# Optimization experiments

Measured on AMD Instinct MI355X. Metric: run time of the kernel, lower is better.

## Reference

```python
import jax, jax.numpy as jnp
import numpy as np

H = 8       # n_heads
N = 128     # n_vars
HEAD = 64   # per-head dim (== __init__ dim)


def setup_inputs() -> dict:
    key = jax.random.key(0)
    k0, k1, k2, k3, k4 = jax.random.split(key, 5)
    B, L = 4, 8192
    D = H * HEAD
    x = jax.random.normal(k0, (B, L, D), dtype=jnp.float32)
    # nn.Linear default init: U(-1/sqrt(fan_in), 1/sqrt(fan_in)), fan_in = HEAD
    s = 1.0 / np.sqrt(HEAD)
    w1 = jax.random.uniform(k1, (HEAD, HEAD), jnp.float32, -s, s)
    b1 = jax.random.uniform(k2, (HEAD,), jnp.float32, -s, s)
    w2 = jax.random.uniform(k3, (HEAD, HEAD), jnp.float32, -s, s)
    b2 = jax.random.uniform(k4, (HEAD,), jnp.float32, -s, s)
    return {"x": x, "w1": w1, "b1": b1, "w2": w2, "b2": b2}


def reference(x, w1, b1, w2, b2):
    B, L, D = x.shape
    P = L // N  # patches per variable
    # (B,L,D) -> (B,H,L,HEAD) -> (B,H,N,P,HEAD)
    xh = x.reshape(B, L, H, HEAD).transpose(0, 2, 1, 3).reshape(B, H, N, P, HEAD)
    q = xh @ w1.T + b1  # proj_1
    k = xh @ w2.T + b2  # proj_2
    # per (b,h,patch) NxN adjacency over variables
    adj = jax.nn.gelu(jnp.einsum('bhixd,bhjxd->bhxij', q, k), approximate=False)
    adj = jax.nn.softmax(adj, axis=-1)
    # dropout is identity in eval mode; F.normalize(p=1): divide by max(L1, eps)
    adj = adj / jnp.maximum(jnp.sum(jnp.abs(adj), axis=-1, keepdims=True), 1e-12)
    out = jnp.einsum('bhxij,bhjxd->bixhd', adj, xh)  # (B,N,P,H,HEAD)
    return out.reshape(B, L, H * HEAD)
```

## Files before the change

kernel.cpp:

```cpp
#include <hip/hip_runtime.h>
#include <math.h>


namespace {
constexpr int H = 8, NV = 128, HEAD = 64, B = 4, L = 8192;
constexpr int P = L / NV;
constexpr int D = H * HEAD;
constexpr int RS = P * D;
constexpr int NT2 = (B * H * P) / 2;

constexpr int XT_S = 136;
constexpr int XH_S = 72;
constexpr int TA_S = 72;

typedef _Float16 half8  __attribute__((ext_vector_type(8)));
typedef _Float16 half4h __attribute__((ext_vector_type(4)));
typedef _Float16 half2v __attribute__((ext_vector_type(2)));
typedef __fp16   fp16x2 __attribute__((ext_vector_type(2)));
typedef float    floatx4 __attribute__((ext_vector_type(4)));

__device__ __forceinline__ floatx4 mfma16(half8 a, half8 b, floatx4 c) {
    return __builtin_amdgcn_mfma_f32_16x16x32_f16(a, b, c, 0, 0, 0);
}

__device__ __forceinline__ half8 cvt8(float4 a, float4 b) {
    fp16x2 p0 = __builtin_amdgcn_cvt_pkrtz(a.x, a.y);
    fp16x2 p1 = __builtin_amdgcn_cvt_pkrtz(a.z, a.w);
    fp16x2 p2 = __builtin_amdgcn_cvt_pkrtz(b.x, b.y);
    fp16x2 p3 = __builtin_amdgcn_cvt_pkrtz(b.z, b.w);
    half8 r;
    r[0] = (_Float16)p0[0]; r[1] = (_Float16)p0[1];
    r[2] = (_Float16)p1[0]; r[3] = (_Float16)p1[1];
    r[4] = (_Float16)p2[0]; r[5] = (_Float16)p2[1];
    r[6] = (_Float16)p3[0]; r[7] = (_Float16)p3[1];
    return r;
}

__device__ __forceinline__ float& vslot(_Float16* xt, int j) {
    return ((float*)(xt + (size_t)(j >> 2) * XT_S + 128))[j & 3];
}

__global__ __launch_bounds__(256) void pack_g(
    const float* __restrict__ w1, const float* __restrict__ w2,
    const float* __restrict__ b1, const float* __restrict__ b2,
    _Float16* __restrict__ gth, float* __restrict__ g1f,
    float* __restrict__ g2f, float* __restrict__ cf)
{
    const int t = threadIdx.x;
    if (blockIdx.x == 16) {
        if (t < 64) {
            float a = 0.f;
            #pragma unroll 8
            for (int n = 0; n < 64; ++n) a = fmaf(w1[n * 64 + t], b2[n], a);
            g1f[t] = a;
        } else if (t < 128) {
            const int d = t - 64;
            float a = 0.f;
            #pragma unroll 8
            for (int n = 0; n < 64; ++n) a = fmaf(w2[n * 64 + d], b1[n], a);
            g2f[d] = a;
        } else if (t == 128) {
            float a = 0.f;
            for (int n = 0; n < 64; ++n) a = fmaf(b1[n], b2[n], a);
            cf[0] = a;
        }
        return;
    }
    const int gid = blockIdx.x * 256 + t;
    const int d = gid & 63, e = gid >> 6;
    float a = 0.f;
    #pragma unroll 8
    for (int n = 0; n < 64; ++n) a = fmaf(w1[n * 64 + d], w2[n * 64 + e], a);
    gth[e * 64 + d] = (_Float16)a;
}

__global__ __launch_bounds__(256, 3) void space_graph_mfma8(
    const float* __restrict__ x, const _Float16* __restrict__ gth,
    const float* __restrict__ g1f, const float* __restrict__ g2f,
    const float* __restrict__ cf, float* __restrict__ out)
{
    __shared__ _Float16 lds[64 * XT_S + NV * XH_S + NV * TA_S];
    _Float16* Xt = lds;
    _Float16* Xh = lds + 64 * XT_S;
    _Float16* TA = Xh + NV * XH_S;

    const int t    = threadIdx.x;
    const int lane = t & 63;
    const int w    = t >> 6;
    const int col  = lane & 15;
    const int quad = lane >> 4;
    const int c    = t & 15;
    const int ttv  = t >> 4;

    const int blk = blockIdx.x;
    const int ti0 = blk, ti1 = blk + NT2;
    const size_t base0 =
        ((size_t)(ti0 >> 9) * L + (size_t)(ti0 & (P - 1))) * D + (size_t)((ti0 >> 6) & (H - 1)) * HEAD;
    const size_t base1 =
        ((size_t)(ti1 >> 9) * L + (size_t)(ti1 & (P - 1))) * D + (size_t)((ti1 >> 6) & (H - 1)) * HEAD;

    float4 pf[8];
    #pragma unroll
    for (int it = 0; it < 4; ++it) {
        const int j0 = 2 * (ttv + 16 * it);
        pf[2 * it]     = *(const float4*)(x + base0 + (size_t)j0 * RS + c * 4);
        pf[2 * it + 1] = *(const float4*)(x + base0 + (size_t)(j0 + 1) * RS + c * 4);
    }

    #pragma unroll
    for (int tile = 0; tile < 2; ++tile) {
        const size_t base = (tile == 0) ? base0 : base1;

        #pragma unroll
        for (int it = 0; it < 4; ++it) {
            const int j0 = 2 * (ttv + 16 * it);
            const float4 v0 = pf[2 * it];
            const float4 v1 = pf[2 * it + 1];
            const float va[4] = {v0.x, v0.y, v0.z, v0.w};
            const float vb[4] = {v1.x, v1.y, v1.z, v1.w};
            half4h ra, rb;
            #pragma unroll
            for (int q = 0; q < 4; ++q) {
                const _Float16 ha = (_Float16)va[q];
                const _Float16 hb = (_Float16)vb[q];
                ra[q] = ha; rb[q] = hb;
                half2v pr; pr[0] = ha; pr[1] = hb;
                *(half2v*)&Xt[(4 * c + q) * XT_S + j0] = pr;
            }
            *(half4h*)&Xh[(size_t)j0 * XH_S + 4 * c] = ra;
            *(half4h*)&Xh[(size_t)(j0 + 1) * XH_S + 4 * c] = rb;
        }

        floatx4 tacc[2][4];
        #pragma unroll
        for (int mt = 0; mt < 2; ++mt)
            #pragma unroll
            for (int nt = 0; nt < 4; ++nt) tacc[mt][nt] = (floatx4)0.0f;

        half8 axf[2][2];
        float up[2] = {0.f, 0.f}, vp[2] = {0.f, 0.f};
        #pragma unroll
        for (int ks = 0; ks < 2; ++ks) {
            const float4 ga = *(const float4*)(g1f + quad * 8 + 32 * ks);
            const float4 gb = *(const float4*)(g1f + quad * 8 + 32 * ks + 4);
            const float4 ha = *(const float4*)(g2f + quad * 8 + 32 * ks);
            const float4 hb = *(const float4*)(g2f + quad * 8 + 32 * ks + 4);
            #pragma unroll
            for (int mt = 0; mt < 2; ++mt) {
                const int row = 32 * w + 16 * mt + col;
                const float* src = x + base + (size_t)row * RS + quad * 8 + 32 * ks;
                const float4 v0 = *(const float4*)src;
                const float4 v1 = *(const float4*)(src + 4);
                axf[mt][ks] = cvt8(v0, v1);
                up[mt] += v0.x * ga.x + v0.y * ga.y + v0.z * ga.z + v0.w * ga.w
                        + v1.x * gb.x + v1.y * gb.y + v1.z * gb.z + v1.w * gb.w;
                vp[mt] += v0.x * ha.x + v0.y * ha.y + v0.z * ha.z + v0.w * ha.w
                        + v1.x * hb.x + v1.y * hb.y + v1.z * hb.z + v1.w * hb.w;
            }
        }

        if (tile == 0) {
            #pragma unroll
            for (int it = 0; it < 4; ++it) {
                const int j0 = 2 * (ttv + 16 * it);
                pf[2 * it]     = *(const float4*)(x + base1 + (size_t)j0 * RS + c * 4);
                pf[2 * it + 1] = *(const float4*)(x + base1 + (size_t)(j0 + 1) * RS + c * 4);
            }
        }

        #pragma unroll
        for (int ks = 0; ks < 2; ++ks)
            #pragma unroll
            for (int nt = 0; nt < 4; ++nt) {
                const half8 gb8 = *(const half8*)&gth[(col + 16 * nt) * HEAD + quad * 8 + 32 * ks];
                #pragma unroll
                for (int mt = 0; mt < 2; ++mt)
                    tacc[mt][nt] = mfma16(axf[mt][ks], gb8, tacc[mt][nt]);
            }

        float ureg[2];
        #pragma unroll
        for (int mt = 0; mt < 2; ++mt) {
            float uu = up[mt]; uu += __shfl_xor(uu, 16); uu += __shfl_xor(uu, 32);
            float vv = vp[mt]; vv += __shfl_xor(vv, 16); vv += __shfl_xor(vv, 32);
            ureg[mt] = uu;
            if (quad == 0) vslot(Xt, 32 * w + 16 * mt + col) = vv;
        }

        #pragma unroll
        for (int mt = 0; mt < 2; ++mt)
            #pragma unroll
            for (int r = 0; r < 4; ++r) {
                const int R = 32 * w + 16 * mt + quad * 4 + r;
                _Float16* trow = &TA[R * TA_S + col];
                #pragma unroll
                for (int nt = 0; nt < 4; ++nt)
                    trow[nt * 16] = (_Float16)(tacc[mt][nt][r]);
            }

        asm volatile("s_waitcnt lgkmcnt(0)" ::: "memory");
        __builtin_amdgcn_s_barrier();
        __builtin_amdgcn_sched_barrier(0);

        const float cc = cf[0];
        float ucr[2][4];
        #pragma unroll
        for (int mt = 0; mt < 2; ++mt)
            #pragma unroll
            for (int r = 0; r < 4; ++r)
                ucr[mt][r] = __shfl(ureg[mt], quad * 4 + r) + cc;
        float vrow[8];
        #pragma unroll
        for (int nt = 0; nt < 8; ++nt) vrow[nt] = vslot(Xt, col + 16 * nt);

        floatx4 sacc[2][8];
        #pragma unroll
        for (int mt = 0; mt < 2; ++mt)
            #pragma unroll
            for (int nt = 0; nt < 8; ++nt)
                #pragma unroll
                for (int r = 0; r < 4; ++r)
                    sacc[mt][nt][r] = ucr[mt][r] + vrow[nt];

        #pragma unroll
        for (int ks = 0; ks < 2; ++ks) {
            half8 taf[2];
            #pragma unroll
            for (int mt = 0; mt < 2; ++mt)
                taf[mt] = *(const half8*)&TA[(32 * w + 16 * mt + col) * TA_S + quad * 8 + 32 * ks];
            #pragma unroll
            for (int nt = 0; nt < 8; ++nt) {
                const half8 xb = *(const half8*)&Xh[(col + 16 * nt) * XH_S + quad * 8 + 32 * ks];
                #pragma unroll
                for (int mt = 0; mt < 2; ++mt)
                    sacc[mt][nt] = mfma16(taf[mt], xb, sacc[mt][nt]);
            }
        }

        #pragma unroll
        for (int mt = 0; mt < 2; ++mt)
            #pragma unroll
            for (int r = 0; r < 4; ++r) {
                float wv[8]; float rs = 0.f;
                #pragma unroll
                for (int nt = 0; nt < 8; ++nt) {
                    const float s  = sacc[mt][nt][r];
                    const float pl = fmaf(s * s, -0.10294310f, -2.3022157f);
                    const float em = __builtin_amdgcn_exp2f(s * pl);
                    const float rr = __builtin_amdgcn_rcpf(1.0f + em);
                    const float e  = __builtin_amdgcn_exp2f((s * 1.44269504f) * rr);
                    wv[nt] = e; rs += e;
                }
                rs += __shfl_xor(rs, 1); rs += __shfl_xor(rs, 2);
                rs += __shfl_xor(rs, 4); rs += __shfl_xor(rs, 8);
                const float inv = __builtin_amdgcn_rcpf(rs);
                #pragma unroll
                for (int nt = 0; nt < 8; ++nt) sacc[mt][nt][r] = wv[nt] * inv;
            }

        #pragma unroll
        for (int mt = 0; mt < 2; ++mt)
            #pragma unroll
            for (int r = 0; r < 4; ++r) {
                const int R = 32 * w + 16 * mt + quad * 4 + r;
                _Float16* arow = &TA[R * TA_S + col];
                #pragma unroll
                for (int nt = 0; nt < 4; ++nt)
                    arow[nt * 16] = (_Float16)(sacc[mt][nt][r]);
            }

        floatx4 oacc[2][4];
        #pragma unroll
        for (int mt = 0; mt < 2; ++mt)
            #pragma unroll
            for (int nt = 0; nt < 4; ++nt) oacc[mt][nt] = (floatx4)0.0f;

        #pragma unroll
        for (int kh = 0; kh < 2; ++kh) {
            half8 aaf[2];
            #pragma unroll
            for (int mt = 0; mt < 2; ++mt)
                aaf[mt] = *(const half8*)&TA[(32 * w + 16 * mt + col) * TA_S + quad * 8 + 32 * kh];
            #pragma unroll
            for (int nt = 0; nt < 4; ++nt) {
                const half8 xb = *(const half8*)&Xt[(col + 16 * nt) * XT_S + quad * 8 + 32 * kh];
                #pragma unroll
                for (int mt = 0; mt < 2; ++mt)
                    oacc[mt][nt] = mfma16(aaf[mt], xb, oacc[mt][nt]);
            }
        }

        #pragma unroll
        for (int mt = 0; mt < 2; ++mt)
            #pragma unroll
            for (int r = 0; r < 4; ++r) {
                const int R = 32 * w + 16 * mt + quad * 4 + r;
                _Float16* arow = &TA[R * TA_S + col];
                #pragma unroll
                for (int nt = 4; nt < 8; ++nt)
                    arow[(nt - 4) * 16] = (_Float16)(sacc[mt][nt][r]);
            }

        #pragma unroll
        for (int kh = 0; kh < 2; ++kh) {
            half8 aaf[2];
            #pragma unroll
            for (int mt = 0; mt < 2; ++mt)
                aaf[mt] = *(const half8*)&TA[(32 * w + 16 * mt + col) * TA_S + quad * 8 + 32 * kh];
            #pragma unroll
            for (int nt = 0; nt < 4; ++nt) {
                const half8 xb = *(const half8*)&Xt[(col + 16 * nt) * XT_S + quad * 8 + 32 * (kh + 2)];
                #pragma unroll
                for (int mt = 0; mt < 2; ++mt)
                    oacc[mt][nt] = mfma16(aaf[mt], xb, oacc[mt][nt]);
            }
        }

        if (tile == 0) __syncthreads();

        #pragma unroll
        for (int mt = 0; mt < 2; ++mt)
            #pragma unroll
            for (int r = 0; r < 4; ++r) {
                const int i = 32 * w + 16 * mt + quad * 4 + r;
                float* orow = out + base + (size_t)i * RS + col;
                #pragma unroll
                for (int nt = 0; nt < 4; ++nt)
                    orow[nt * 16] = oacc[mt][nt][r];
            }
    }
}
}

extern "C" void kernel_launch(void* const* d_in, const int* in_sizes, int n_in,
                              void* d_out, int out_size, void* d_ws, size_t ws_size,
                              hipStream_t stream) {
    const float* x  = (const float*)d_in[0];
    const float* w1 = (const float*)d_in[1];
    const float* b1 = (const float*)d_in[2];
    const float* w2 = (const float*)d_in[3];
    const float* b2 = (const float*)d_in[4];
    float* out = (float*)d_out;

    _Float16* gth = (_Float16*)d_ws;
    float* g1f = (float*)((char*)d_ws + 8192);
    float* g2f = g1f + 64;
    float* cf  = g2f + 64;

    hipLaunchKernelGGL(pack_g, dim3(17), dim3(256), 0, stream,
                       w1, w2, b1, b2, gth, g1f, g2f, cf);
    hipLaunchKernelGGL(space_graph_mfma8, dim3(NT2), dim3(256), 0, stream,
                       x, gth, g1f, g2f, cf, out);
}
```

Before: 156.2 us.

## Fold bias-term vectors into MFMA tile and read A operand from LDS

The row/column bias projections (u and v) are now computed as a fifth MFMA output tile by appending the two bias vectors as extra rows of the packed G matrix, replacing the scalar FMA dot products and cross-lane shuffles. The A operand is read from the already-staged half-precision LDS copy instead of reloading x from global memory and converting it. This removes redundant global reads and scalar work, but adds extra block barriers and a zero-padded fifth MFMA column group, and computes the bias dot products in fp16.

```diff
diff --git a/kernel.cpp b/kernel.cpp
--- a/kernel.cpp
+++ b/kernel.cpp
@@ -16,49 +16,38 @@
 typedef _Float16 half8  __attribute__((ext_vector_type(8)));
 typedef _Float16 half4h __attribute__((ext_vector_type(4)));
 typedef _Float16 half2v __attribute__((ext_vector_type(2)));
-typedef __fp16   fp16x2 __attribute__((ext_vector_type(2)));
 typedef float    floatx4 __attribute__((ext_vector_type(4)));
 
 __device__ __forceinline__ floatx4 mfma16(half8 a, half8 b, floatx4 c) {
     return __builtin_amdgcn_mfma_f32_16x16x32_f16(a, b, c, 0, 0, 0);
 }
 
-__device__ __forceinline__ half8 cvt8(float4 a, float4 b) {
-    fp16x2 p0 = __builtin_amdgcn_cvt_pkrtz(a.x, a.y);
-    fp16x2 p1 = __builtin_amdgcn_cvt_pkrtz(a.z, a.w);
-    fp16x2 p2 = __builtin_amdgcn_cvt_pkrtz(b.x, b.y);
-    fp16x2 p3 = __builtin_amdgcn_cvt_pkrtz(b.z, b.w);
-    half8 r;
-    r[0] = (_Float16)p0[0]; r[1] = (_Float16)p0[1];
-    r[2] = (_Float16)p1[0]; r[3] = (_Float16)p1[1];
-    r[4] = (_Float16)p2[0]; r[5] = (_Float16)p2[1];
-    r[6] = (_Float16)p3[0]; r[7] = (_Float16)p3[1];
-    return r;
-}
-
+__device__ __forceinline__ float& uslot(_Float16* xt, int j) {
+    return ((float*)(xt + (j >> 2) * XT_S + 128))[j & 3];
+}
 __device__ __forceinline__ float& vslot(_Float16* xt, int j) {
-    return ((float*)(xt + (size_t)(j >> 2) * XT_S + 128))[j & 3];
+    return ((float*)(xt + (32 + (j >> 2)) * XT_S + 128))[j & 3];
 }
 
 __global__ __launch_bounds__(256) void pack_g(
     const float* __restrict__ w1, const float* __restrict__ w2,
     const float* __restrict__ b1, const float* __restrict__ b2,
-    _Float16* __restrict__ gth, float* __restrict__ g1f,
-    float* __restrict__ g2f, float* __restrict__ cf)
+    _Float16* __restrict__ gxh, float* __restrict__ cf)
 {
     const int t = threadIdx.x;
     if (blockIdx.x == 16) {
+        for (int z = t; z < 14 * 64; z += 256) gxh[66 * 64 + z] = (_Float16)0.f;
         if (t < 64) {
             float a = 0.f;
             #pragma unroll 8
-            for (int n = 0; n < 64; ++n) a = fmaf(w1[n * 64 + t], b2[n], a);
-            g1f[t] = a;
+            for (int n = 0; n < 64; ++n) a = fmaf(w2[n * 64 + t], b1[n], a);
+            gxh[64 * 64 + t] = (_Float16)a;
         } else if (t < 128) {
             const int d = t - 64;
             float a = 0.f;
             #pragma unroll 8
-            for (int n = 0; n < 64; ++n) a = fmaf(w2[n * 64 + d], b1[n], a);
-            g2f[d] = a;
+            for (int n = 0; n < 64; ++n) a = fmaf(w1[n * 64 + d], b2[n], a);
+            gxh[65 * 64 + d] = (_Float16)a;
         } else if (t == 128) {
             float a = 0.f;
             for (int n = 0; n < 64; ++n) a = fmaf(b1[n], b2[n], a);
@@ -71,12 +60,11 @@
     float a = 0.f;
     #pragma unroll 8
     for (int n = 0; n < 64; ++n) a = fmaf(w1[n * 64 + d], w2[n * 64 + e], a);
-    gth[e * 64 + d] = (_Float16)a;
-}
-
-__global__ __launch_bounds__(256, 3) void space_graph_mfma8(
-    const float* __restrict__ x, const _Float16* __restrict__ gth,
-    const float* __restrict__ g1f, const float* __restrict__ g2f,
+    gxh[e * 64 + d] = (_Float16)a;
+}
+
+__global__ __launch_bounds__(256, 3) void space_graph_mfma9(
+    const float* __restrict__ x, const _Float16* __restrict__ gxh,
     const float* __restrict__ cf, float* __restrict__ out)
 {
     __shared__ _Float16 lds[64 * XT_S + NV * XH_S + NV * TA_S];
@@ -99,6 +87,8 @@
     const size_t base1 =
         ((size_t)(ti1 >> 9) * L + (size_t)(ti1 & (P - 1))) * D + (size_t)((ti1 >> 6) & (H - 1)) * HEAD;
 
+    const float cc = cf[0];
+
     float4 pf[8];
     #pragma unroll
     for (int it = 0; it < 4; ++it) {
@@ -111,6 +101,12 @@
     for (int tile = 0; tile < 2; ++tile) {
         const size_t base = (tile == 0) ? base0 : base1;
 
+        if (tile == 1) {
+            asm volatile("s_waitcnt lgkmcnt(0)" ::: "memory");
+            __builtin_amdgcn_s_barrier();
+            __builtin_amdgcn_sched_barrier(0);
+        }
+
         #pragma unroll
         for (int it = 0; it < 4; ++it) {
             const int j0 = 2 * (ttv + 16 * it);
@@ -131,33 +127,56 @@
             *(half4h*)&Xh[(size_t)(j0 + 1) * XH_S + 4 * c] = rb;
         }
 
-        floatx4 tacc[2][4];
-        #pragma unroll
-        for (int mt = 0; mt < 2; ++mt)
-            #pragma unroll
-            for (int nt = 0; nt < 4; ++nt) tacc[mt][nt] = (floatx4)0.0f;
+        asm volatile("s_waitcnt lgkmcnt(0)" ::: "memory");
+        __builtin_amdgcn_s_barrier();
+        __builtin_amdgcn_sched_barrier(0);
+
+        floatx4 tacc[2][5];
+        #pragma unroll
+        for (int mt = 0; mt < 2; ++mt)
+            #pragma unroll
+            for (int nt = 0; nt < 5; ++nt) tacc[mt][nt] = (floatx4)0.0f;
 
         half8 axf[2][2];
-        float up[2] = {0.f, 0.f}, vp[2] = {0.f, 0.f};
-        #pragma unroll
-        for (int ks = 0; ks < 2; ++ks) {
-            const float4 ga = *(const float4*)(g1f + quad * 8 + 32 * ks);
-            const float4 gb = *(const float4*)(g1f + quad * 8 + 32 * ks + 4);
-            const float4 ha = *(const float4*)(g2f + quad * 8 + 32 * ks);
-            const float4 hb = *(const float4*)(g2f + quad * 8 + 32 * ks + 4);
-            #pragma unroll
-            for (int mt = 0; mt < 2; ++mt) {
-                const int row = 32 * w + 16 * mt + col;
-                const float* src = x + base + (size_t)row * RS + quad * 8 + 32 * ks;
-                const float4 v0 = *(const float4*)src;
-                const float4 v1 = *(const float4*)(src + 4);
-                axf[mt][ks] = cvt8(v0, v1);
-                up[mt] += v0.x * ga.x + v0.y * ga.y + v0.z * ga.z + v0.w * ga.w
-                        + v1.x * gb.x + v1.y * gb.y + v1.z * gb.z + v1.w * gb.w;
-                vp[mt] += v0.x * ha.x + v0.y * ha.y + v0.z * ha.z + v0.w * ha.w
-                        + v1.x * hb.x + v1.y * hb.y + v1.z * hb.z + v1.w * hb.w;
-            }
-        }
+        #pragma unroll
+        for (int ks = 0; ks < 2; ++ks)
+            #pragma unroll
+            for (int mt = 0; mt < 2; ++mt)
+                axf[mt][ks] = *(const half8*)&Xh[(32 * w + 16 * mt + col) * XH_S + quad * 8 + 32 * ks];
+
+        #pragma unroll
+        for (int ks = 0; ks < 2; ++ks)
+            #pragma unroll
+            for (int nt = 0; nt < 5; ++nt) {
+                const half8 gb8 = *(const half8*)&gxh[(col + 16 * nt) * HEAD + quad * 8 + 32 * ks];
+                #pragma unroll
+                for (int mt = 0; mt < 2; ++mt)
+                    tacc[mt][nt] = mfma16(axf[mt][ks], gb8, tacc[mt][nt]);
+            }
+
+        #pragma unroll
+        for (int mt = 0; mt < 2; ++mt)
+            #pragma unroll
+            for (int r = 0; r < 4; ++r) {
+                const int R = 32 * w + 16 * mt + quad * 4 + r;
+                if (col == 0) vslot(Xt, R) = tacc[mt][4][r];
+                if (col == 1) uslot(Xt, R) = tacc[mt][4][r];
+            }
+
+        #pragma unroll
+        for (int mt = 0; mt < 2; ++mt)
+            #pragma unroll
+            for (int r = 0; r < 4; ++r) {
+                const int R = 32 * w + 16 * mt + quad * 4 + r;
+                _Float16* trow = &TA[R * TA_S + col];
+                #pragma unroll
+                for (int nt = 0; nt < 4; ++nt)
+                    trow[nt * 16] = (_Float16)(tacc[mt][nt][r]);
+            }
+
+        asm volatile("s_waitcnt lgkmcnt(0)" ::: "memory");
+        __builtin_amdgcn_s_barrier();
+        __builtin_amdgcn_sched_barrier(0);
 
         if (tile == 0) {
             #pragma unroll
@@ -166,49 +185,15 @@
                 pf[2 * it]     = *(const float4*)(x + base1 + (size_t)j0 * RS + c * 4);
                 pf[2 * it + 1] = *(const float4*)(x + base1 + (size_t)(j0 + 1) * RS + c * 4);
             }
-        }
-
-        #pragma unroll
-        for (int ks = 0; ks < 2; ++ks)
-            #pragma unroll
-            for (int nt = 0; nt < 4; ++nt) {
-                const half8 gb8 = *(const half8*)&gth[(col + 16 * nt) * HEAD + quad * 8 + 32 * ks];
-                #pragma unroll
-                for (int mt = 0; mt < 2; ++mt)
-                    tacc[mt][nt] = mfma16(axf[mt][ks], gb8, tacc[mt][nt]);
-            }
-
-        float ureg[2];
-        #pragma unroll
-        for (int mt = 0; mt < 2; ++mt) {
-            float uu = up[mt]; uu += __shfl_xor(uu, 16); uu += __shfl_xor(uu, 32);
-            float vv = vp[mt]; vv += __shfl_xor(vv, 16); vv += __shfl_xor(vv, 32);
-            ureg[mt] = uu;
-            if (quad == 0) vslot(Xt, 32 * w + 16 * mt + col) = vv;
-        }
-
-        #pragma unroll
-        for (int mt = 0; mt < 2; ++mt)
-            #pragma unroll
-            for (int r = 0; r < 4; ++r) {
-                const int R = 32 * w + 16 * mt + quad * 4 + r;
-                _Float16* trow = &TA[R * TA_S + col];
-                #pragma unroll
-                for (int nt = 0; nt < 4; ++nt)
-                    trow[nt * 16] = (_Float16)(tacc[mt][nt][r]);
-            }
-
-        asm volatile("s_waitcnt lgkmcnt(0)" ::: "memory");
-        __builtin_amdgcn_s_barrier();
-        __builtin_amdgcn_sched_barrier(0);
-
-        const float cc = cf[0];
+            __builtin_amdgcn_sched_barrier(0);
+        }
+
         float ucr[2][4];
         #pragma unroll
         for (int mt = 0; mt < 2; ++mt)
             #pragma unroll
             for (int r = 0; r < 4; ++r)
-                ucr[mt][r] = __shfl(ureg[mt], quad * 4 + r) + cc;
+                ucr[mt][r] = uslot(Xt, 32 * w + 16 * mt + quad * 4 + r) + cc;
         float vrow[8];
         #pragma unroll
         for (int nt = 0; nt < 8; ++nt) vrow[nt] = vslot(Xt, col + 16 * nt);
@@ -316,8 +301,6 @@
             }
         }
 
-        if (tile == 0) __syncthreads();
-
         #pragma unroll
         for (int mt = 0; mt < 2; ++mt)
             #pragma unroll
@@ -342,13 +325,11 @@
     const float* b2 = (const float*)d_in[4];
     float* out = (float*)d_out;
 
-    _Float16* gth = (_Float16*)d_ws;
-    float* g1f = (float*)((char*)d_ws + 8192);
-    float* g2f = g1f + 64;
-    float* cf  = g2f + 64;
+    _Float16* gxh = (_Float16*)d_ws;
+    float* cf = (float*)((char*)d_ws + 10240);
 
     hipLaunchKernelGGL(pack_g, dim3(17), dim3(256), 0, stream,
-                       w1, w2, b1, b2, gth, g1f, g2f, cf);
-    hipLaunchKernelGGL(space_graph_mfma8, dim3(NT2), dim3(256), 0, stream,
-                       x, gth, g1f, g2f, cf, out);
-}
+                       w1, w2, b1, b2, gxh, cf);
+    hipLaunchKernelGGL(space_graph_mfma9, dim3(NT2), dim3(256), 0, stream,
+                       x, gxh, cf, out);
+}
```

Result: no change. 158.7 us (+1.6%).
